# Kernel tuning notes

Measured on AMD Instinct MI355X. Metric: run time of the kernel, lower is better.

## Reference

```python
import jax, jax.numpy as jnp
import numpy as np

N = 65536
EMB_DIM = 1024
PICK_NUM = 12  # ceil(ln(65536)) = ceil(11.09) = 12


def setup_inputs() -> dict:
    key = jax.random.key(0)
    k_emb, k_wq, k_bq, k_wk, k_bk, k_idx = jax.random.split(key, 6)
    s = 1.0 / np.sqrt(EMB_DIM)
    embed_matrix = jax.random.normal(k_emb, (N, EMB_DIM), dtype=jnp.float32)
    Wq = jax.random.normal(k_wq, (EMB_DIM, EMB_DIM), dtype=jnp.float32) * s
    bq = jax.random.normal(k_bq, (EMB_DIM,), dtype=jnp.float32) * s
    Wk = jax.random.normal(k_wk, (EMB_DIM, EMB_DIM), dtype=jnp.float32) * s
    bk = jax.random.normal(k_bk, (EMB_DIM,), dtype=jnp.float32) * s
    # np.random.choice(n, pick_num, replace=False) -> deterministic permutation slice
    indices = jax.random.permutation(k_idx, N)[:PICK_NUM].astype(jnp.int32)
    return {"embed_matrix": embed_matrix, "Wq": Wq, "bq": bq,
            "Wk": Wk, "bk": bk, "indices": indices}


def reference(embed_matrix, Wq, bq, Wk, bk, indices):
    pick_num = indices.shape[0]
    # torch.nn.Linear: y = x @ W.T + b
    query = embed_matrix @ Wq.T + bq          # [n, d]
    key = embed_matrix @ Wk.T + bk            # [n, d]
    new_key = key[indices]                    # [pick, d] sampled keys
    Q_K_sample = query @ new_key.T            # [n, pick]
    max_values = jnp.max(Q_K_sample, axis=1)  # [n]
    _, top_indices = jax.lax.top_k(max_values, pick_num)
    Q_reduced = query[top_indices]            # [pick, d]
    Q_K = Q_reduced @ key.T                   # [pick, n]
    pooled = jnp.max(Q_K, axis=0, keepdims=True)  # [1, n]
    attention_embed = pooled @ embed_matrix   # [1, d]
    return attention_embed
```

## Files before the change

kernel.cpp:

```cpp
#include <hip/hip_runtime.h>

#define DIM 1024
#define NROWS 65536
#define PICK 12


__global__ void __launch_bounds__(256)
rows12_kernel(const float* __restrict__ emb, const float* __restrict__ W,
              const float* __restrict__ b, const int* __restrict__ idx,
              float* __restrict__ out) {
    int d = blockIdx.x;
    int t = threadIdx.x;
    int lane = t & 63;
    int q = t >> 6;
    int e0 = q * 256 + lane * 4;
    float4 w4 = *(const float4*)&W[(size_t)d * DIM + e0];
    float part[PICK];
#pragma unroll
    for (int j = 0; j < PICK; ++j) {
        int r = idx[j];
        float4 e4 = *(const float4*)&emb[(size_t)r * DIM + e0];
        part[j] = w4.x * e4.x + w4.y * e4.y + w4.z * e4.z + w4.w * e4.w;
    }
#pragma unroll
    for (int j = 0; j < PICK; ++j) {
        float v = part[j];
        for (int s = 32; s > 0; s >>= 1) v += __shfl_down(v, s, 64);
        part[j] = v;
    }
    __shared__ float red[4][PICK];
    if (lane == 0) {
#pragma unroll
        for (int j = 0; j < PICK; ++j) red[q][j] = part[j];
    }
    __syncthreads();
    if (t < PICK) {
        float s = red[0][t] + red[1][t] + red[2][t] + red[3][t] + b[d];
        out[t * DIM + d] = s;
    }
}

__global__ void __launch_bounds__(256)
colmat_kernel(const float* __restrict__ W, const float* __restrict__ V,
              const float* __restrict__ b, float* __restrict__ out,
              float* __restrict__ cvec) {
    int blk = blockIdx.x;
    int t = threadIdx.x;
    if (blk == 128) {
        float part[PICK];
#pragma unroll
        for (int j = 0; j < PICK; ++j) part[j] = 0.f;
        for (int k = 0; k < 4; ++k) {
            int d = t + k * 256;
            float bv = b[d];
#pragma unroll
            for (int j = 0; j < PICK; ++j) part[j] += bv * V[j * DIM + d];
        }
#pragma unroll
        for (int j = 0; j < PICK; ++j) {
            float v = part[j];
            for (int s = 32; s > 0; s >>= 1) v += __shfl_down(v, s, 64);
            if ((t & 63) == 0) atomicAdd(&cvec[j], v);
        }
        return;
    }
    int eg = blk & 3;
    int dg = blk >> 2;
    int e = eg * 256 + t;
    int d0 = dg * 32;
    __shared__ float Vs[PICK][32];
    for (int i = t; i < PICK * 32; i += 256) {
        int j = i >> 5, dd = i & 31;
        Vs[j][dd] = V[j * DIM + d0 + dd];
    }
    __syncthreads();
    float acc[PICK];
#pragma unroll
    for (int j = 0; j < PICK; ++j) acc[j] = 0.f;
    for (int dd = 0; dd < 32; ++dd) {
        float w = W[(size_t)(d0 + dd) * DIM + e];
#pragma unroll
        for (int j = 0; j < PICK; ++j) acc[j] += w * Vs[j][dd];
    }
#pragma unroll
    for (int j = 0; j < PICK; ++j) atomicAdd(&out[e * PICK + j], acc[j]);
}


__global__ void __launch_bounds__(512)
pass1_kernel(const float* __restrict__ emb, const float* __restrict__ M,
             const float* __restrict__ c0, float* __restrict__ maxv) {
    __shared__ float sM[DIM * PICK];
    int t = threadIdx.x;
    for (int i = t; i < DIM * PICK / 4; i += 512)
        ((float4*)sM)[i] = ((const float4*)M)[i];
    __syncthreads();

    int l = t & 63, w = t >> 6;
    int g = l >> 2, s = l & 3;
    size_t row = (size_t)blockIdx.x * 128 + w * 16 + g;
    const float* rp = emb + row * DIM + s * 4;
    float cb[PICK];
#pragma unroll
    for (int j = 0; j < PICK; ++j) cb[j] = c0[j];

    float acc[PICK];
#pragma unroll
    for (int j = 0; j < PICK; ++j) acc[j] = 0.f;
    float4 cur = *(const float4*)rp;
#pragma unroll 4
    for (int i = 0; i < 64; ++i) {
        float4 nxt = *(const float4*)(rp + (i + 1 < 64 ? i + 1 : i) * 16);
        const float* mb = sM + (size_t)(i * 16 + s * 4) * PICK;
        float f[4] = {cur.x, cur.y, cur.z, cur.w};
#pragma unroll
        for (int x = 0; x < 4; ++x) {
            float4 m0 = *(const float4*)(mb + x * PICK + 0);
            float4 m1 = *(const float4*)(mb + x * PICK + 4);
            float4 m2 = *(const float4*)(mb + x * PICK + 8);
            acc[0] += f[x] * m0.x; acc[1] += f[x] * m0.y;
            acc[2] += f[x] * m0.z; acc[3] += f[x] * m0.w;
            acc[4] += f[x] * m1.x; acc[5] += f[x] * m1.y;
            acc[6] += f[x] * m1.z; acc[7] += f[x] * m1.w;
            acc[8] += f[x] * m2.x; acc[9] += f[x] * m2.y;
            acc[10] += f[x] * m2.z; acc[11] += f[x] * m2.w;
        }
        cur = nxt;
    }
#pragma unroll
    for (int j = 0; j < PICK; ++j) {
        acc[j] += __shfl_xor(acc[j], 1, 64);
        acc[j] += __shfl_xor(acc[j], 2, 64);
    }
    float mx = acc[0] + cb[0];
#pragma unroll
    for (int j = 1; j < PICK; ++j) mx = fmaxf(mx, acc[j] + cb[j]);
    if (s == 0) maxv[row] = mx;
}

__global__ void __launch_bounds__(512)
pass2_kernel(const float* __restrict__ emb, const float* __restrict__ Rt,
             const float* __restrict__ c1, float* __restrict__ out) {
    __shared__ float sM[DIM * PICK];
    __shared__ float pooled[8][16];
    __shared__ float obuf[2][DIM];
    int t = threadIdx.x;
    for (int i = t; i < DIM * PICK / 4; i += 512)
        ((float4*)sM)[i] = ((const float4*)Rt)[i];
    __syncthreads();

    int l = t & 63, w = t >> 6;
    int g = l >> 2, s = l & 3;
    size_t rbase = (size_t)blockIdx.x * 128 + w * 16;
    size_t row = rbase + g;
    const float* rp = emb + row * DIM + s * 4;
    float cb[PICK];
#pragma unroll
    for (int j = 0; j < PICK; ++j) cb[j] = c1[j];

    float acc[PICK];
#pragma unroll
    for (int j = 0; j < PICK; ++j) acc[j] = 0.f;
    float4 cur = *(const float4*)rp;
#pragma unroll 4
    for (int i = 0; i < 64; ++i) {
        float4 nxt = *(const float4*)(rp + (i + 1 < 64 ? i + 1 : i) * 16);
        const float* mb = sM + (size_t)(i * 16 + s * 4) * PICK;
        float f[4] = {cur.x, cur.y, cur.z, cur.w};
#pragma unroll
        for (int x = 0; x < 4; ++x) {
            float4 m0 = *(const float4*)(mb + x * PICK + 0);
            float4 m1 = *(const float4*)(mb + x * PICK + 4);
            float4 m2 = *(const float4*)(mb + x * PICK + 8);
            acc[0] += f[x] * m0.x; acc[1] += f[x] * m0.y;
            acc[2] += f[x] * m0.z; acc[3] += f[x] * m0.w;
            acc[4] += f[x] * m1.x; acc[5] += f[x] * m1.y;
            acc[6] += f[x] * m1.z; acc[7] += f[x] * m1.w;
            acc[8] += f[x] * m2.x; acc[9] += f[x] * m2.y;
            acc[10] += f[x] * m2.z; acc[11] += f[x] * m2.w;
        }
        cur = nxt;
    }
#pragma unroll
    for (int j = 0; j < PICK; ++j) {
        acc[j] += __shfl_xor(acc[j], 1, 64);
        acc[j] += __shfl_xor(acc[j], 2, 64);
    }
    float mx = acc[0] + cb[0];
#pragma unroll
    for (int j = 1; j < PICK; ++j) mx = fmaxf(mx, acc[j] + cb[j]);
    if (s == 0) pooled[w][g] = mx;

    float o[4][4];
#pragma unroll
    for (int c = 0; c < 4; ++c)
#pragma unroll
        for (int x = 0; x < 4; ++x) o[c][x] = 0.f;
    const float* tp = emb + rbase * DIM + l * 4;
    for (int r = 0; r < 16; ++r) {
        float p = pooled[w][r];
#pragma unroll
        for (int c = 0; c < 4; ++c) {
            float4 v = *(const float4*)(tp + (size_t)r * DIM + c * 256);
            o[c][0] += p * v.x; o[c][1] += p * v.y;
            o[c][2] += p * v.z; o[c][3] += p * v.w;
        }
    }
    for (int ph = 0; ph < 4; ++ph) {
        if ((w >> 1) == ph) {
            float* ob = obuf[w & 1];
            if (ph == 0) {
#pragma unroll
                for (int c = 0; c < 4; ++c)
                    *(float4*)(ob + c * 256 + l * 4) = *(float4*)o[c];
            } else {
#pragma unroll
                for (int c = 0; c < 4; ++c) {
                    float4 prev = *(float4*)(ob + c * 256 + l * 4);
                    prev.x += o[c][0]; prev.y += o[c][1];
                    prev.z += o[c][2]; prev.w += o[c][3];
                    *(float4*)(ob + c * 256 + l * 4) = prev;
                }
            }
        }
        __syncthreads();
    }
    for (int c = t; c < DIM; c += 512)
        atomicAdd(&out[c], obuf[0][c] + obuf[1][c]);
}

__global__ void __launch_bounds__(256)
top12_local(const float* __restrict__ maxv, float* __restrict__ cand_v,
            int* __restrict__ cand_i) {
    int t = threadIdx.x;
    int base = blockIdx.x * 1024;
    __shared__ float mv[1024];
    __shared__ float sv[256];
    __shared__ int si[256];
    for (int i = t; i < 1024; i += 256) mv[i] = maxv[base + i];
    __syncthreads();
    for (int k = 0; k < PICK; ++k) {
        float bv = -3e38f; int bi = 0x7fffffff;
        for (int i = t; i < 1024; i += 256) {
            float v = mv[i];
            if (v > bv || (v == bv && base + i < bi)) { bv = v; bi = base + i; }
        }
        sv[t] = bv; si[t] = bi;
        __syncthreads();
        for (int s = 128; s > 0; s >>= 1) {
            if (t < s) {
                if (sv[t + s] > sv[t] || (sv[t + s] == sv[t] && si[t + s] < si[t])) {
                    sv[t] = sv[t + s]; si[t] = si[t + s];
                }
            }
            __syncthreads();
        }
        if (t == 0) {
            cand_v[blockIdx.x * PICK + k] = sv[0];
            cand_i[blockIdx.x * PICK + k] = si[0];
            mv[si[0] - base] = -3e38f;
        }
        __syncthreads();
    }
}

__global__ void __launch_bounds__(256)
top12_merge(const float* __restrict__ cand_v, const int* __restrict__ cand_i,
            int* __restrict__ top_idx) {
    int t = threadIdx.x;
    __shared__ float mv[768];
    __shared__ int mi[768];
    __shared__ float sv[256];
    __shared__ int si[256];
    __shared__ int sl[256];
    for (int i = t; i < 768; i += 256) { mv[i] = cand_v[i]; mi[i] = cand_i[i]; }
    __syncthreads();
    for (int k = 0; k < PICK; ++k) {
        float bv = -3e38f; int bi = 0x7fffffff; int bl = -1;
        for (int i = t; i < 768; i += 256) {
            float v = mv[i]; int ii = mi[i];
            if (v > bv || (v == bv && ii < bi)) { bv = v; bi = ii; bl = i; }
        }
        sv[t] = bv; si[t] = bi; sl[t] = bl;
        __syncthreads();
        for (int s = 128; s > 0; s >>= 1) {
            if (t < s) {
                if (sv[t + s] > sv[t] || (sv[t + s] == sv[t] && si[t + s] < si[t])) {
                    sv[t] = sv[t + s]; si[t] = si[t + s]; sl[t] = sl[t + s];
                }
            }
            __syncthreads();
        }
        if (t == 0) { top_idx[k] = si[0]; mv[sl[0]] = -3e38f; }
        __syncthreads();
    }
}

extern "C" void kernel_launch(void* const* d_in, const int* in_sizes, int n_in,
                              void* d_out, int out_size, void* d_ws, size_t ws_size,
                              hipStream_t stream) {
    const float* emb = (const float*)d_in[0];
    const float* Wq  = (const float*)d_in[1];
    const float* bq  = (const float*)d_in[2];
    const float* Wk  = (const float*)d_in[3];
    const float* bk  = (const float*)d_in[4];
    const int* indices = (const int*)d_in[5];
    float* out = (float*)d_out;
    float* ws = (float*)d_ws;

    float* NK      = ws;
    float* Qr      = ws + 12288;
    float* M       = ws + 24576;
    float* Rt      = ws + 36864;
    float* c0      = ws + 49152;
    float* c1      = ws + 49168;
    float* cand_v  = ws + 49184;
    int*   cand_i  = (int*)(ws + 49952);
    int*   top_idx = (int*)(ws + 50720);
    float* maxv    = ws + 50736;

    hipMemsetAsync(M, 0, (size_t)(12288 * 2 + 32) * sizeof(float), stream);
    hipMemsetAsync(out, 0, DIM * sizeof(float), stream);

    rows12_kernel<<<1024, 256, 0, stream>>>(emb, Wk, bk, indices, NK);
    colmat_kernel<<<129, 256, 0, stream>>>(Wq, NK, bq, M, c0);
    pass1_kernel<<<512, 512, 0, stream>>>(emb, M, c0, maxv);
    top12_local<<<64, 256, 0, stream>>>(maxv, cand_v, cand_i);
    top12_merge<<<1, 256, 0, stream>>>(cand_v, cand_i, top_idx);
    rows12_kernel<<<1024, 256, 0, stream>>>(emb, Wq, bq, top_idx, Qr);
    colmat_kernel<<<129, 256, 0, stream>>>(Wk, Qr, bk, Rt, c1);
    pass2_kernel<<<512, 512, 0, stream>>>(emb, Rt, c1, out);
}
```

Before: 606.8 us.

## Process four rows per thread in streaming passes to reuse shared-memory projection loads

Each thread in pass1 and pass2 now accumulates four rows at once, so every shared-memory load of the 12-column projection matrix is reused across four embedding rows instead of one. Blocks shrink to 256 threads covering 256 rows, and the grid drops to 256 blocks. Pass2's weighted sum becomes a simple per-thread loop over all 256 block rows, with direct atomics and no phased shared-memory reduction. The cost is higher register pressure (48 accumulators plus 12 float4 matrix values), fewer resident waves to hide memory latency, and a grid of 256 blocks that may underfill the GPU.

```diff
diff --git a/kernel.cpp b/kernel.cpp
--- a/kernel.cpp
+++ b/kernel.cpp
@@ -87,146 +87,168 @@
 }
 
 
-__global__ void __launch_bounds__(512)
+__global__ void __launch_bounds__(256)
 pass1_kernel(const float* __restrict__ emb, const float* __restrict__ M,
              const float* __restrict__ c0, float* __restrict__ maxv) {
     __shared__ float sM[DIM * PICK];
     int t = threadIdx.x;
-    for (int i = t; i < DIM * PICK / 4; i += 512)
+    for (int i = t; i < DIM * PICK / 4; i += 256)
         ((float4*)sM)[i] = ((const float4*)M)[i];
     __syncthreads();
 
     int l = t & 63, w = t >> 6;
     int g = l >> 2, s = l & 3;
-    size_t row = (size_t)blockIdx.x * 128 + w * 16 + g;
-    const float* rp = emb + row * DIM + s * 4;
+    size_t wbase = (size_t)blockIdx.x * 256 + w * 64;
+    const float* rp[4];
+    float4 cur[4];
+#pragma unroll
+    for (int rr = 0; rr < 4; ++rr) {
+        rp[rr] = emb + (wbase + rr * 16 + g) * DIM + s * 4;
+        cur[rr] = *(const float4*)rp[rr];
+    }
     float cb[PICK];
 #pragma unroll
     for (int j = 0; j < PICK; ++j) cb[j] = c0[j];
 
-    float acc[PICK];
-#pragma unroll
-    for (int j = 0; j < PICK; ++j) acc[j] = 0.f;
-    float4 cur = *(const float4*)rp;
-#pragma unroll 4
+    float acc[4][PICK];
+#pragma unroll
+    for (int rr = 0; rr < 4; ++rr)
+#pragma unroll
+        for (int j = 0; j < PICK; ++j) acc[rr][j] = 0.f;
+
     for (int i = 0; i < 64; ++i) {
-        float4 nxt = *(const float4*)(rp + (i + 1 < 64 ? i + 1 : i) * 16);
+        int ip = (i + 1 < 64) ? i + 1 : i;
+        float4 nxt[4];
+#pragma unroll
+        for (int rr = 0; rr < 4; ++rr) nxt[rr] = *(const float4*)(rp[rr] + ip * 16);
         const float* mb = sM + (size_t)(i * 16 + s * 4) * PICK;
-        float f[4] = {cur.x, cur.y, cur.z, cur.w};
-#pragma unroll
-        for (int x = 0; x < 4; ++x) {
-            float4 m0 = *(const float4*)(mb + x * PICK + 0);
-            float4 m1 = *(const float4*)(mb + x * PICK + 4);
-            float4 m2 = *(const float4*)(mb + x * PICK + 8);
-            acc[0] += f[x] * m0.x; acc[1] += f[x] * m0.y;
-            acc[2] += f[x] * m0.z; acc[3] += f[x] * m0.w;
-            acc[4] += f[x] * m1.x; acc[5] += f[x] * m1.y;
-            acc[6] += f[x] * m1.z; acc[7] += f[x] * m1.w;
-            acc[8] += f[x] * m2.x; acc[9] += f[x] * m2.y;
-            acc[10] += f[x] * m2.z; acc[11] += f[x] * m2.w;
-        }
-        cur = nxt;
-    }
-#pragma unroll
-    for (int j = 0; j < PICK; ++j) {
-        acc[j] += __shfl_xor(acc[j], 1, 64);
-        acc[j] += __shfl_xor(acc[j], 2, 64);
-    }
-    float mx = acc[0] + cb[0];
-#pragma unroll
-    for (int j = 1; j < PICK; ++j) mx = fmaxf(mx, acc[j] + cb[j]);
-    if (s == 0) maxv[row] = mx;
-}
-
-__global__ void __launch_bounds__(512)
+        float4 m[12];
+#pragma unroll
+        for (int k = 0; k < 12; ++k) m[k] = *(const float4*)(mb + k * 4);
+#pragma unroll
+        for (int rr = 0; rr < 4; ++rr) {
+            float f[4] = {cur[rr].x, cur[rr].y, cur[rr].z, cur[rr].w};
+#pragma unroll
+            for (int x = 0; x < 4; ++x) {
+                float4 a0 = m[3 * x], a1 = m[3 * x + 1], a2 = m[3 * x + 2];
+                acc[rr][0] += f[x] * a0.x; acc[rr][1] += f[x] * a0.y;
+                acc[rr][2] += f[x] * a0.z; acc[rr][3] += f[x] * a0.w;
+                acc[rr][4] += f[x] * a1.x; acc[rr][5] += f[x] * a1.y;
+                acc[rr][6] += f[x] * a1.z; acc[rr][7] += f[x] * a1.w;
+                acc[rr][8] += f[x] * a2.x; acc[rr][9] += f[x] * a2.y;
+                acc[rr][10] += f[x] * a2.z; acc[rr][11] += f[x] * a2.w;
+            }
+        }
+#pragma unroll
+        for (int rr = 0; rr < 4; ++rr) cur[rr] = nxt[rr];
+    }
+#pragma unroll
+    for (int rr = 0; rr < 4; ++rr)
+#pragma unroll
+        for (int j = 0; j < PICK; ++j) {
+            acc[rr][j] += __shfl_xor(acc[rr][j], 1, 64);
+            acc[rr][j] += __shfl_xor(acc[rr][j], 2, 64);
+        }
+    float mx[4];
+#pragma unroll
+    for (int rr = 0; rr < 4; ++rr) {
+        float v = acc[rr][0] + cb[0];
+#pragma unroll
+        for (int j = 1; j < PICK; ++j) v = fmaxf(v, acc[rr][j] + cb[j]);
+        mx[rr] = v;
+    }
+    float sel = (s == 0) ? mx[0] : (s == 1) ? mx[1] : (s == 2) ? mx[2] : mx[3];
+    maxv[wbase + s * 16 + g] = sel;
+}
+
+__global__ void __launch_bounds__(256)
 pass2_kernel(const float* __restrict__ emb, const float* __restrict__ Rt,
              const float* __restrict__ c1, float* __restrict__ out) {
     __shared__ float sM[DIM * PICK];
-    __shared__ float pooled[8][16];
-    __shared__ float obuf[2][DIM];
-    int t = threadIdx.x;
-    for (int i = t; i < DIM * PICK / 4; i += 512)
+    __shared__ float pooled[256];
+    int t = threadIdx.x;
+    for (int i = t; i < DIM * PICK / 4; i += 256)
         ((float4*)sM)[i] = ((const float4*)Rt)[i];
     __syncthreads();
 
     int l = t & 63, w = t >> 6;
     int g = l >> 2, s = l & 3;
-    size_t rbase = (size_t)blockIdx.x * 128 + w * 16;
-    size_t row = rbase + g;
-    const float* rp = emb + row * DIM + s * 4;
+    size_t bbase = (size_t)blockIdx.x * 256;
+    size_t wbase = bbase + w * 64;
+    const float* rp[4];
+    float4 cur[4];
+#pragma unroll
+    for (int rr = 0; rr < 4; ++rr) {
+        rp[rr] = emb + (wbase + rr * 16 + g) * DIM + s * 4;
+        cur[rr] = *(const float4*)rp[rr];
+    }
     float cb[PICK];
 #pragma unroll
     for (int j = 0; j < PICK; ++j) cb[j] = c1[j];
 
-    float acc[PICK];
-#pragma unroll
-    for (int j = 0; j < PICK; ++j) acc[j] = 0.f;
-    float4 cur = *(const float4*)rp;
-#pragma unroll 4
+    float acc[4][PICK];
+#pragma unroll
+    for (int rr = 0; rr < 4; ++rr)
+#pragma unroll
+        for (int j = 0; j < PICK; ++j) acc[rr][j] = 0.f;
+
     for (int i = 0; i < 64; ++i) {
-        float4 nxt = *(const float4*)(rp + (i + 1 < 64 ? i + 1 : i) * 16);
+        int ip = (i + 1 < 64) ? i + 1 : i;
+        float4 nxt[4];
+#pragma unroll
+        for (int rr = 0; rr < 4; ++rr) nxt[rr] = *(const float4*)(rp[rr] + ip * 16);
         const float* mb = sM + (size_t)(i * 16 + s * 4) * PICK;
-        float f[4] = {cur.x, cur.y, cur.z, cur.w};
-#pragma unroll
-        for (int x = 0; x < 4; ++x) {
-            float4 m0 = *(const float4*)(mb + x * PICK + 0);
-            float4 m1 = *(const float4*)(mb + x * PICK + 4);
-            float4 m2 = *(const float4*)(mb + x * PICK + 8);
-            acc[0] += f[x] * m0.x; acc[1] += f[x] * m0.y;
-            acc[2] += f[x] * m0.z; acc[3] += f[x] * m0.w;
-            acc[4] += f[x] * m1.x; acc[5] += f[x] * m1.y;
-            acc[6] += f[x] * m1.z; acc[7] += f[x] * m1.w;
-            acc[8] += f[x] * m2.x; acc[9] += f[x] * m2.y;
-            acc[10] += f[x] * m2.z; acc[11] += f[x] * m2.w;
-        }
-        cur = nxt;
-    }
-#pragma unroll
-    for (int j = 0; j < PICK; ++j) {
-        acc[j] += __shfl_xor(acc[j], 1, 64);
-        acc[j] += __shfl_xor(acc[j], 2, 64);
-    }
-    float mx = acc[0] + cb[0];
-#pragma unroll
-    for (int j = 1; j < PICK; ++j) mx = fmaxf(mx, acc[j] + cb[j]);
-    if (s == 0) pooled[w][g] = mx;
-
-    float o[4][4];
-#pragma unroll
-    for (int c = 0; c < 4; ++c)
-#pragma unroll
-        for (int x = 0; x < 4; ++x) o[c][x] = 0.f;
-    const float* tp = emb + rbase * DIM + l * 4;
-    for (int r = 0; r < 16; ++r) {
-        float p = pooled[w][r];
-#pragma unroll
-        for (int c = 0; c < 4; ++c) {
-            float4 v = *(const float4*)(tp + (size_t)r * DIM + c * 256);
-            o[c][0] += p * v.x; o[c][1] += p * v.y;
-            o[c][2] += p * v.z; o[c][3] += p * v.w;
-        }
-    }
-    for (int ph = 0; ph < 4; ++ph) {
-        if ((w >> 1) == ph) {
-            float* ob = obuf[w & 1];
-            if (ph == 0) {
-#pragma unroll
-                for (int c = 0; c < 4; ++c)
-                    *(float4*)(ob + c * 256 + l * 4) = *(float4*)o[c];
-            } else {
-#pragma unroll
-                for (int c = 0; c < 4; ++c) {
-                    float4 prev = *(float4*)(ob + c * 256 + l * 4);
-                    prev.x += o[c][0]; prev.y += o[c][1];
-                    prev.z += o[c][2]; prev.w += o[c][3];
-                    *(float4*)(ob + c * 256 + l * 4) = prev;
-                }
+        float4 m[12];
+#pragma unroll
+        for (int k = 0; k < 12; ++k) m[k] = *(const float4*)(mb + k * 4);
+#pragma unroll
+        for (int rr = 0; rr < 4; ++rr) {
+            float f[4] = {cur[rr].x, cur[rr].y, cur[rr].z, cur[rr].w};
+#pragma unroll
+            for (int x = 0; x < 4; ++x) {
+                float4 a0 = m[3 * x], a1 = m[3 * x + 1], a2 = m[3 * x + 2];
+                acc[rr][0] += f[x] * a0.x; acc[rr][1] += f[x] * a0.y;
+                acc[rr][2] += f[x] * a0.z; acc[rr][3] += f[x] * a0.w;
+                acc[rr][4] += f[x] * a1.x; acc[rr][5] += f[x] * a1.y;
+                acc[rr][6] += f[x] * a1.z; acc[rr][7] += f[x] * a1.w;
+                acc[rr][8] += f[x] * a2.x; acc[rr][9] += f[x] * a2.y;
+                acc[rr][10] += f[x] * a2.z; acc[rr][11] += f[x] * a2.w;
             }
         }
-        __syncthreads();
-    }
-    for (int c = t; c < DIM; c += 512)
-        atomicAdd(&out[c], obuf[0][c] + obuf[1][c]);
+#pragma unroll
+        for (int rr = 0; rr < 4; ++rr) cur[rr] = nxt[rr];
+    }
+#pragma unroll
+    for (int rr = 0; rr < 4; ++rr)
+#pragma unroll
+        for (int j = 0; j < PICK; ++j) {
+            acc[rr][j] += __shfl_xor(acc[rr][j], 1, 64);
+            acc[rr][j] += __shfl_xor(acc[rr][j], 2, 64);
+        }
+    float mx[4];
+#pragma unroll
+    for (int rr = 0; rr < 4; ++rr) {
+        float v = acc[rr][0] + cb[0];
+#pragma unroll
+        for (int j = 1; j < PICK; ++j) v = fmaxf(v, acc[rr][j] + cb[j]);
+        mx[rr] = v;
+    }
+    float sel = (s == 0) ? mx[0] : (s == 1) ? mx[1] : (s == 2) ? mx[2] : mx[3];
+    pooled[w * 64 + s * 16 + g] = sel;
+    __syncthreads();
+
+    const float* tp = emb + bbase * DIM + t * 4;
+    float4 o = {0.f, 0.f, 0.f, 0.f};
+#pragma unroll 8
+    for (int r = 0; r < 256; ++r) {
+        float p = pooled[r];
+        float4 v = *(const float4*)(tp + (size_t)r * DIM);
+        o.x += p * v.x; o.y += p * v.y; o.z += p * v.z; o.w += p * v.w;
+    }
+    atomicAdd(&out[t * 4 + 0], o.x);
+    atomicAdd(&out[t * 4 + 1], o.y);
+    atomicAdd(&out[t * 4 + 2], o.z);
+    atomicAdd(&out[t * 4 + 3], o.w);
 }
 
 __global__ void __launch_bounds__(256)
@@ -324,10 +346,10 @@
 
     rows12_kernel<<<1024, 256, 0, stream>>>(emb, Wk, bk, indices, NK);
     colmat_kernel<<<129, 256, 0, stream>>>(Wq, NK, bq, M, c0);
-    pass1_kernel<<<512, 512, 0, stream>>>(emb, M, c0, maxv);
+    pass1_kernel<<<256, 256, 0, stream>>>(emb, M, c0, maxv);
     top12_local<<<64, 256, 0, stream>>>(maxv, cand_v, cand_i);
     top12_merge<<<1, 256, 0, stream>>>(cand_v, cand_i, top_idx);
     rows12_kernel<<<1024, 256, 0, stream>>>(emb, Wq, bq, top_idx, Qr);
     colmat_kernel<<<129, 256, 0, stream>>>(Wk, Qr, bk, Rt, c1);
-    pass2_kernel<<<512, 512, 0, stream>>>(emb, Rt, c1, out);
-}
+    pass2_kernel<<<256, 256, 0, stream>>>(emb, Rt, c1, out);
+}
```

Result: faster. 594.7 us (-2.0%).
